# Optimization experiments

Hardware: AMD Instinct MI355X
Metric: run time of the kernel (lower is better)

Reference implementation:

```python
import jax, jax.numpy as jnp
import numpy as np

DIM = 1024
HID = 2048
E = 8      # num_experts
K = 2      # num_experts_per_tok
R = 16     # lora_rank
B_, S_ = 2, 1024


def setup_inputs() -> dict:
    key = jax.random.key(0)
    ks = jax.random.split(key, 14)
    n = lambda k, shape, scale: jax.random.normal(k, shape, jnp.float32) * scale
    inp = {
        "x": jax.random.normal(ks[0], (B_, S_, DIM), jnp.float32),
        "Wg": n(ks[1], (E, DIM), DIM ** -0.5),
        # w1: dim -> hidden (base weight, bias, lora A [r,in], lora B [out,r])
        "W1": n(ks[2], (E, HID, DIM), DIM ** -0.5),
        "b1": jnp.zeros((E, HID), jnp.float32),
        "A1": n(ks[3], (E, R, DIM), DIM ** -0.5),
        "B1": n(ks[4], (E, HID, R), 0.01),
        # w2: hidden -> dim
        "W2": n(ks[5], (E, DIM, HID), HID ** -0.5),
        "b2": jnp.zeros((E, DIM), jnp.float32),
        "A2": n(ks[6], (E, R, HID), HID ** -0.5),
        "B2": n(ks[7], (E, DIM, R), 0.01),
        # w3: dim -> hidden
        "W3": n(ks[8], (E, HID, DIM), DIM ** -0.5),
        "b3": jnp.zeros((E, HID), jnp.float32),
        "A3": n(ks[9], (E, R, DIM), DIM ** -0.5),
        "B3": n(ks[10], (E, HID, R), 0.01),
    }
    return inp


def _lora_in(xf, W, b, A, B):
    # xf: [T, D] shared input -> [T, E, H]; LoraLinear: x W^T + b + (x A^T) B^T
    base = jnp.einsum('td,ehd->teh', xf, W)
    low = jnp.einsum('ter,ehr->teh', jnp.einsum('td,erd->ter', xf, A), B)
    return base + low + b


def _lora_out(g, W, b, A, B):
    # g: [T, E, H] per-expert input -> [T, E, D]
    base = jnp.einsum('teh,edh->ted', g, W)
    low = jnp.einsum('ter,edr->ted', jnp.einsum('teh,erh->ter', g, A), B)
    return base + low + b


def reference(x, Wg, W1, b1, A1, B1, W2, b2, A2, B2, W3, b3, A3, B3):
    orig_shape = x.shape
    xf = x.reshape(-1, x.shape[-1])                      # [T, D]
    scores = jax.nn.softmax(xf @ Wg.T, axis=-1)          # [T, E]
    expert_weights, expert_indices = jax.lax.top_k(scores, K)
    expert_weights = expert_weights / expert_weights.sum(-1, keepdims=True)
    # sparse combine weights: zero for non-topk experts (== masked dispatch)
    gates = (jax.nn.one_hot(expert_indices, E, dtype=xf.dtype)
             * expert_weights[..., None]).sum(axis=1)    # [T, E]
    h1 = _lora_in(xf, W1, b1, A1, B1)                    # [T, E, H]
    h3 = _lora_in(xf, W3, b3, A3, B3)                    # [T, E, H]
    g = jax.nn.silu(h1) * h3                             # silu gating
    y_e = _lora_out(g, W2, b2, A2, B2)                   # [T, E, D]
    y = jnp.einsum('te,ted->td', gates, y_e)             # weighted combine
    return y.reshape(orig_shape)
```

## Files before the change

kernel.cpp:

```cpp
#include <hip/hip_runtime.h>

#define DIM 1024
#define HID 2048
#define NE 8
#define LR 16
#define T_TOK 2048
#define NROWS 4096
#define BM 128
#define BN 64
#define BK 64
#define MAX_MT 40
#define ROWS_PAD (NROWS + BM)

typedef __attribute__((ext_vector_type(8))) short bf16x8;
typedef __attribute__((ext_vector_type(4))) float f32x4;

__device__ __forceinline__ unsigned short f2bf(float f) {
  unsigned u = __builtin_bit_cast(unsigned, f);
  u += 0x7FFFu + ((u >> 16) & 1u);
  return (unsigned short)(u >> 16);
}

__device__ __forceinline__ void gload_lds16(const void* g, void* l) {
  __builtin_amdgcn_global_load_lds(
      (const __attribute__((address_space(1))) unsigned int*)g,
      (__attribute__((address_space(3))) unsigned int*)l, 16, 0, 0);
}

__global__ void routing_kernel(const float* __restrict__ x, const float* __restrict__ Wg,
                               int* __restrict__ counts, int* __restrict__ topk_idx,
                               float* __restrict__ topk_gate) {
  int t = blockIdx.x * 4 + (threadIdx.x >> 6);
  int lane = threadIdx.x & 63;
  const float* xr = x + (size_t)t * DIM;
  float xa[16];
#pragma unroll
  for (int i = 0; i < 16; i++) xa[i] = xr[lane + 64 * i];
  float lg[NE];
#pragma unroll
  for (int e = 0; e < NE; e++) {
    const float* wr_ = Wg + e * DIM;
    float s = 0.f;
#pragma unroll
    for (int i = 0; i < 16; i++) s += xa[i] * wr_[lane + 64 * i];
#pragma unroll
    for (int off = 32; off > 0; off >>= 1) s += __shfl_xor(s, off);
    lg[e] = s;
  }
  if (lane == 0) {
    int i0 = 0;
#pragma unroll
    for (int e = 1; e < NE; e++) if (lg[e] > lg[i0]) i0 = e;
    int i1 = (i0 == 0) ? 1 : 0;
#pragma unroll
    for (int e = 0; e < NE; e++) if (e != i0 && lg[e] > lg[i1]) i1 = e;
    float e1 = __expf(lg[i1] - lg[i0]);
    float inv = 1.f / (1.f + e1);
    topk_idx[2 * t] = i0;
    topk_idx[2 * t + 1] = i1;
    topk_gate[2 * t] = inv;
    topk_gate[2 * t + 1] = e1 * inv;
    atomicAdd(&counts[i0], 1);
    atomicAdd(&counts[i1], 1);
  }
}

__global__ void scan_kernel(const int* __restrict__ counts, int* __restrict__ offsets,
                            int* __restrict__ nmt, int* __restrict__ tiles) {
  if (threadIdx.x == 0) {
    int off = 0, nt = 0;
    for (int e = 0; e < NE; e++) {
      offsets[e] = off;
      int c = counts[e];
      for (int mm = 0; mm * BM < c; mm++) tiles[nt++] = (e << 16) | mm;
      off += c;
    }
    offsets[NE] = off;
    nmt[0] = nt;
  }
}

__global__ void scatter_kernel(const int* __restrict__ topk_idx,
                               const int* __restrict__ offsets, int* __restrict__ cursors,
                               int* __restrict__ perm, int* __restrict__ rowexp,
                               int* __restrict__ pos) {
  int i = blockIdx.x * 256 + threadIdx.x;
  int e = topk_idx[i];
  int r = offsets[e] + atomicAdd(&cursors[e], 1);
  perm[r] = i >> 1;
  rowexp[r] = e;
  pos[i] = r;
}

__global__ void gather_lora13_kernel(const float* __restrict__ x,
                                     const float* __restrict__ A1, const float* __restrict__ A3,
                                     const int* __restrict__ perm, const int* __restrict__ rowexp,
                                     unsigned short* __restrict__ Xg,
                                     float* __restrict__ t1g, float* __restrict__ t3g) {
  __shared__ float xs[DIM];
  int r = blockIdx.x;
  int t = perm[r], e = rowexp[r];
  int tid = threadIdx.x;
  float4 v = ((const float4*)(x + (size_t)t * DIM))[tid];
  ((float4*)xs)[tid] = v;
  ushort4 hv;
  hv.x = f2bf(v.x); hv.y = f2bf(v.y); hv.z = f2bf(v.z); hv.w = f2bf(v.w);
  ((ushort4*)(Xg + (size_t)r * DIM))[tid] = hv;
  __syncthreads();
  int w = tid >> 6, lane = tid & 63;
  const float* A = ((w < 2) ? A1 : A3) + (size_t)e * LR * DIM + (size_t)((w & 1) * 8) * DIM;
  float* tout = ((w < 2) ? t1g : t3g) + (size_t)r * LR + (w & 1) * 8;
  float acc[8];
#pragma unroll
  for (int j = 0; j < 8; j++) acc[j] = 0.f;
  for (int i = 0; i < 16; i++) {
    float xv = xs[lane + 64 * i];
#pragma unroll
    for (int j = 0; j < 8; j++) acc[j] += xv * A[(size_t)j * DIM + lane + 64 * i];
  }
#pragma unroll
  for (int j = 0; j < 8; j++) {
    float s = acc[j];
#pragma unroll
    for (int off = 32; off > 0; off >>= 1) s += __shfl_xor(s, off);
    if (lane == 0) tout[j] = s;
  }
}

__global__ void lora2_kernel(const unsigned short* __restrict__ gb,
                             const float* __restrict__ A2, const int* __restrict__ rowexp,
                             float* __restrict__ t2g) {
  __shared__ float gs[HID];
  int r = blockIdx.x, tid = threadIdx.x;
  int e = rowexp[r];
  uint4 raw = ((const uint4*)(gb + (size_t)r * HID))[tid];
  unsigned u[4] = {raw.x, raw.y, raw.z, raw.w};
#pragma unroll
  for (int k = 0; k < 4; k++) {
    gs[tid * 8 + 2 * k] = __builtin_bit_cast(float, u[k] << 16);
    gs[tid * 8 + 2 * k + 1] = __builtin_bit_cast(float, u[k] & 0xffff0000u);
  }
  __syncthreads();
  int w = tid >> 6, lane = tid & 63;
  const float* A = A2 + (size_t)e * LR * HID + (size_t)(w * 4) * HID;
  float acc[4];
#pragma unroll
  for (int j = 0; j < 4; j++) acc[j] = 0.f;
  for (int i = 0; i < HID / 64; i++) {
    float xv = gs[lane + 64 * i];
#pragma unroll
    for (int j = 0; j < 4; j++) acc[j] += xv * A[(size_t)j * HID + lane + 64 * i];
  }
#pragma unroll
  for (int j = 0; j < 4; j++) {
    float s = acc[j];
#pragma unroll
    for (int off = 32; off > 0; off >>= 1) s += __shfl_xor(s, off);
    if (lane == 0) t2g[(size_t)r * LR + w * 4 + j] = s;
  }
}

__global__ __launch_bounds__(256) void gemm1_dual(
    const unsigned short* __restrict__ Xg,
    const float* __restrict__ W1, const float* __restrict__ W3,
    const float* __restrict__ b1, const float* __restrict__ b3,
    const float* __restrict__ B1l, const float* __restrict__ B3l,
    const float* __restrict__ t1g, const float* __restrict__ t3g,
    const int* __restrict__ offsets, const int* __restrict__ nmt,
    const int* __restrict__ tiles,
    unsigned short* __restrict__ g) {
  int ntid = blockIdx.x & 31;
  int slot = blockIdx.x >> 5;
  if (slot >= nmt[0]) return;
  int tl = tiles[slot];
  int e = tl >> 16, mtile = tl & 0xffff;
  int row0 = offsets[e] + mtile * BM;
  int rowEnd = offsets[e + 1];
  int col0 = ntid * BN;

  __shared__ __align__(16) char smem[32768];
  unsigned short* As = (unsigned short*)smem;
  unsigned short* B1s = (unsigned short*)(smem + 16384);
  unsigned short* B3s = (unsigned short*)(smem + 24576);

  int tid = threadIdx.x, lane = tid & 63, w = tid >> 6;
  int wr = w >> 1, wc = w & 1;

  f32x4 acc1[4][2], acc3[4][2];
#pragma unroll
  for (int i = 0; i < 4; i++)
#pragma unroll
    for (int j = 0; j < 2; j++)
#pragma unroll
      for (int k = 0; k < 4; k++) { acc1[i][j][k] = 0.f; acc3[i][j][k] = 0.f; }

  const unsigned short* Ag = Xg + (size_t)row0 * DIM;
  const float* W1e = W1 + ((size_t)e * HID + col0) * DIM;
  const float* W3e = W3 + ((size_t)e * HID + col0) * DIM;

  for (int kt = 0; kt < DIM / BK; kt++) {
#pragma unroll
    for (int it = 0; it < 4; it++) {
      int rl = it * 32 + w * 8 + (lane >> 3);
      int cb = (lane & 7) * 8;
      gload_lds16(Ag + (size_t)rl * DIM + kt * BK + cb, As + (it * 32 + w * 8) * BK);
    }
#pragma unroll
    for (int it = 0; it < 4; it++) {
      int rl = it * 16 + (tid >> 4);
      int cs = (tid & 15) * 4;
      float4 f1 = *(const float4*)(W1e + (size_t)rl * DIM + kt * BK + cs);
      float4 f3 = *(const float4*)(W3e + (size_t)rl * DIM + kt * BK + cs);
      ushort4 h1, h3;
      h1.x = f2bf(f1.x); h1.y = f2bf(f1.y); h1.z = f2bf(f1.z); h1.w = f2bf(f1.w);
      h3.x = f2bf(f3.x); h3.y = f2bf(f3.y); h3.z = f2bf(f3.z); h3.w = f2bf(f3.w);
      *(ushort4*)(B1s + rl * BK + cs) = h1;
      *(ushort4*)(B3s + rl * BK + cs) = h3;
    }
    __syncthreads();
#pragma unroll
    for (int kk = 0; kk < 2; kk++) {
      bf16x8 a[4];
#pragma unroll
      for (int mm = 0; mm < 4; mm++)
        a[mm] = *(const bf16x8*)(As + (wr * 64 + mm * 16 + (lane & 15)) * BK + kk * 32 + (lane >> 4) * 8);
#pragma unroll
      for (int nn = 0; nn < 2; nn++) {
        bf16x8 bv1 = *(const bf16x8*)(B1s + (wc * 32 + nn * 16 + (lane & 15)) * BK + kk * 32 + (lane >> 4) * 8);
        bf16x8 bv3 = *(const bf16x8*)(B3s + (wc * 32 + nn * 16 + (lane & 15)) * BK + kk * 32 + (lane >> 4) * 8);
#pragma unroll
        for (int mm = 0; mm < 4; mm++) {
          acc1[mm][nn] = __builtin_amdgcn_mfma_f32_16x16x32_bf16(a[mm], bv1, acc1[mm][nn], 0, 0, 0);
          acc3[mm][nn] = __builtin_amdgcn_mfma_f32_16x16x32_bf16(a[mm], bv3, acc3[mm][nn], 0, 0, 0);
        }
      }
    }
    __syncthreads();
  }

  float* sT1 = (float*)smem;
  float* sT3 = sT1 + 128 * 17;
  float* sC1 = sT3 + 128 * 17;
  float* sC3 = sC1 + 64 * 17;
  float* sb1 = sC3 + 64 * 17;
  float* sb3 = sb1 + 64;
  for (int i = tid; i < 128 * 16; i += 256) {
    int rr = i >> 4, jj = i & 15;
    sT1[rr * 17 + jj] = t1g[(size_t)(row0 + rr) * LR + jj];
    sT3[rr * 17 + jj] = t3g[(size_t)(row0 + rr) * LR + jj];
  }
  for (int i = tid; i < 64 * 16; i += 256) {
    int rr = i >> 4, jj = i & 15;
    sC1[rr * 17 + jj] = B1l[((size_t)e * HID + col0 + rr) * LR + jj];
    sC3[rr * 17 + jj] = B3l[((size_t)e * HID + col0 + rr) * LR + jj];
  }
  if (tid < 64) {
    sb1[tid] = b1[e * HID + col0 + tid];
    sb3[tid] = b3[e * HID + col0 + tid];
  }
  __syncthreads();
#pragma unroll
  for (int mm = 0; mm < 4; mm++)
#pragma unroll
    for (int nn = 0; nn < 2; nn++) {
      int cl = wc * 32 + nn * 16 + (lane & 15);
      float bias1 = sb1[cl], bias3 = sb3[cl];
#pragma unroll
      for (int j = 0; j < 4; j++) {
        int rl = wr * 64 + mm * 16 + (lane >> 4) * 4 + j;
        float v1 = acc1[mm][nn][j] + bias1;
        float v3 = acc3[mm][nn][j] + bias3;
#pragma unroll
        for (int jj = 0; jj < 16; jj++) {
          v1 += sT1[rl * 17 + jj] * sC1[cl * 17 + jj];
          v3 += sT3[rl * 17 + jj] * sC3[cl * 17 + jj];
        }
        float gg = v1 * v3 / (1.f + __expf(-v1));
        int r = row0 + rl;
        if (r < rowEnd) g[(size_t)r * HID + col0 + cl] = f2bf(gg);
      }
    }
}

__global__ __launch_bounds__(256) void gemm2_kernel(
    const unsigned short* __restrict__ gb,
    const float* __restrict__ W2, const float* __restrict__ b2,
    const float* __restrict__ B2l, const float* __restrict__ t2g,
    const int* __restrict__ offsets, const int* __restrict__ nmt,
    const int* __restrict__ tiles,
    float* __restrict__ ye) {
  int ntid = blockIdx.x & 15;
  int slot = blockIdx.x >> 4;
  if (slot >= nmt[0]) return;
  int tl = tiles[slot];
  int e = tl >> 16, mtile = tl & 0xffff;
  int row0 = offsets[e] + mtile * BM;
  int rowEnd = offsets[e + 1];
  int col0 = ntid * BN;

  __shared__ __align__(16) char smem[24576];
  unsigned short* As = (unsigned short*)smem;
  unsigned short* Bs = (unsigned short*)(smem + 16384);

  int tid = threadIdx.x, lane = tid & 63, w = tid >> 6;
  int wr = w >> 1, wc = w & 1;

  f32x4 acc[4][2];
#pragma unroll
  for (int i = 0; i < 4; i++)
#pragma unroll
    for (int j = 0; j < 2; j++)
#pragma unroll
      for (int k = 0; k < 4; k++) acc[i][j][k] = 0.f;

  const unsigned short* Ag = gb + (size_t)row0 * HID;
  const float* W2e = W2 + ((size_t)e * DIM + col0) * HID;

  for (int kt = 0; kt < HID / BK; kt++) {
#pragma unroll
    for (int it = 0; it < 4; it++) {
      int rl = it * 32 + w * 8 + (lane >> 3);
      int cb = (lane & 7) * 8;
      gload_lds16(Ag + (size_t)rl * HID + kt * BK + cb, As + (it * 32 + w * 8) * BK);
    }
#pragma unroll
    for (int it = 0; it < 4; it++) {
      int rl = it * 16 + (tid >> 4);
      int cs = (tid & 15) * 4;
      float4 f = *(const float4*)(W2e + (size_t)rl * HID + kt * BK + cs);
      ushort4 h;
      h.x = f2bf(f.x); h.y = f2bf(f.y); h.z = f2bf(f.z); h.w = f2bf(f.w);
      *(ushort4*)(Bs + rl * BK + cs) = h;
    }
    __syncthreads();
#pragma unroll
    for (int kk = 0; kk < 2; kk++) {
      bf16x8 a[4];
#pragma unroll
      for (int mm = 0; mm < 4; mm++)
        a[mm] = *(const bf16x8*)(As + (wr * 64 + mm * 16 + (lane & 15)) * BK + kk * 32 + (lane >> 4) * 8);
#pragma unroll
      for (int nn = 0; nn < 2; nn++) {
        bf16x8 bv = *(const bf16x8*)(Bs + (wc * 32 + nn * 16 + (lane & 15)) * BK + kk * 32 + (lane >> 4) * 8);
#pragma unroll
        for (int mm = 0; mm < 4; mm++)
          acc[mm][nn] = __builtin_amdgcn_mfma_f32_16x16x32_bf16(a[mm], bv, acc[mm][nn], 0, 0, 0);
      }
    }
    __syncthreads();
  }

  float* sT2 = (float*)smem;
  float* sC2 = sT2 + 128 * 17;
  float* sb2 = sC2 + 64 * 17;
  for (int i = tid; i < 128 * 16; i += 256) {
    int rr = i >> 4, jj = i & 15;
    sT2[rr * 17 + jj] = t2g[(size_t)(row0 + rr) * LR + jj];
  }
  for (int i = tid; i < 64 * 16; i += 256) {
    int rr = i >> 4, jj = i & 15;
    sC2[rr * 17 + jj] = B2l[((size_t)e * DIM + col0 + rr) * LR + jj];
  }
  if (tid < 64) sb2[tid] = b2[e * DIM + col0 + tid];
  __syncthreads();
#pragma unroll
  for (int mm = 0; mm < 4; mm++)
#pragma unroll
    for (int nn = 0; nn < 2; nn++) {
      int cl = wc * 32 + nn * 16 + (lane & 15);
      float bias = sb2[cl];
#pragma unroll
      for (int j = 0; j < 4; j++) {
        int rl = wr * 64 + mm * 16 + (lane >> 4) * 4 + j;
        float v = acc[mm][nn][j] + bias;
#pragma unroll
        for (int jj = 0; jj < 16; jj++) v += sT2[rl * 17 + jj] * sC2[cl * 17 + jj];
        int r = row0 + rl;
        if (r < rowEnd) ye[(size_t)r * DIM + col0 + cl] = v;
      }
    }
}

__global__ void combine_kernel(const float* __restrict__ ye, const int* __restrict__ pos,
                               const float* __restrict__ topk_gate,
                               float* __restrict__ out) {
  int t = blockIdx.x, tid = threadIdx.x;
  int r0 = pos[2 * t], r1 = pos[2 * t + 1];
  float w0 = topk_gate[2 * t], w1 = topk_gate[2 * t + 1];
  float4 a = ((const float4*)(ye + (size_t)r0 * DIM))[tid];
  float4 b = ((const float4*)(ye + (size_t)r1 * DIM))[tid];
  float4 o;
  o.x = w0 * a.x + w1 * b.x;
  o.y = w0 * a.y + w1 * b.y;
  o.z = w0 * a.z + w1 * b.z;
  o.w = w0 * a.w + w1 * b.w;
  ((float4*)(out + (size_t)t * DIM))[tid] = o;
}

extern "C" void kernel_launch(void* const* d_in, const int* in_sizes, int n_in,
                              void* d_out, int out_size, void* d_ws, size_t ws_size,
                              hipStream_t stream) {
  (void)in_sizes; (void)n_in; (void)out_size; (void)ws_size;
  const float* x  = (const float*)d_in[0];
  const float* Wg = (const float*)d_in[1];
  const float* W1 = (const float*)d_in[2];
  const float* b1 = (const float*)d_in[3];
  const float* A1 = (const float*)d_in[4];
  const float* B1 = (const float*)d_in[5];
  const float* W2 = (const float*)d_in[6];
  const float* b2 = (const float*)d_in[7];
  const float* A2 = (const float*)d_in[8];
  const float* B2 = (const float*)d_in[9];
  const float* W3 = (const float*)d_in[10];
  const float* b3 = (const float*)d_in[11];
  const float* A3 = (const float*)d_in[12];
  const float* B3 = (const float*)d_in[13];
  float* out = (float*)d_out;

  char* ws = (char*)d_ws;
  int* counts   = (int*)ws;
  int* cursors  = counts + 8;
  int* offsets  = cursors + 8;
  int* nmt      = offsets + 9;
  int* tiles    = nmt + 1;
  int* topk_idx = (int*)(ws + 512);
  float* topk_gate = (float*)(ws + 512 + 16384);
  int* perm   = (int*)(ws + 512 + 2 * 16384);
  int* rowexp = (int*)(ws + 512 + 3 * 16384);
  int* pos    = (int*)(ws + 512 + 4 * 16384);
  size_t off = 82432;
  unsigned short* Xg = (unsigned short*)(ws + off); off += (size_t)ROWS_PAD * DIM * 2;
  unsigned short* gb = (unsigned short*)(ws + off); off += (size_t)ROWS_PAD * HID * 2;
  float* t1g = (float*)(ws + off); off += (size_t)ROWS_PAD * LR * 4;
  float* t3g = (float*)(ws + off); off += (size_t)ROWS_PAD * LR * 4;
  float* t2g = (float*)(ws + off); off += (size_t)ROWS_PAD * LR * 4;
  float* ye  = (float*)(ws + off); off += (size_t)NROWS * DIM * 4;

  hipMemsetAsync(d_ws, 0, 512, stream);
  routing_kernel<<<T_TOK / 4, 256, 0, stream>>>(x, Wg, counts, topk_idx, topk_gate);
  scan_kernel<<<1, 64, 0, stream>>>(counts, offsets, nmt, tiles);
  scatter_kernel<<<NROWS / 256, 256, 0, stream>>>(topk_idx, offsets, cursors, perm, rowexp, pos);
  gather_lora13_kernel<<<NROWS, 256, 0, stream>>>(x, A1, A3, perm, rowexp, Xg, t1g, t3g);
  gemm1_dual<<<MAX_MT * (HID / BN), 256, 0, stream>>>(Xg, W1, W3, b1, b3, B1, B3, t1g, t3g,
                                                      offsets, nmt, tiles, gb);
  lora2_kernel<<<NROWS, 256, 0, stream>>>(gb, A2, rowexp, t2g);
  gemm2_kernel<<<MAX_MT * (DIM / BN), 256, 0, stream>>>(gb, W2, b2, B2, t2g,
                                                        offsets, nmt, tiles, ye);
  combine_kernel<<<T_TOK, 256, 0, stream>>>(ye, pos, topk_gate, out);
}
```

Baseline: 690.1 us.

## Pre-convert expert weights to bf16 and double-buffer swizzled LDS loads in GEMMs

Adds a conversion kernel that turns W1, W3 and W2 into bf16 copies in the workspace every call. The two expert GEMMs can then stream weights directly into LDS with global_load_lds instead of converting them in registers. Both GEMMs become double-buffered with an XOR swizzle on the LDS layout, so the next tile loads while the current one computes and bank conflicts drop. The cost is an extra full read and write pass over all three weight tensors each call, plus twice the LDS per block, which may lower occupancy.

```diff
diff --git a/kernel.cpp b/kernel.cpp
--- a/kernel.cpp
+++ b/kernel.cpp
@@ -11,6 +11,7 @@
 #define BK 64
 #define MAX_MT 40
 #define ROWS_PAD (NROWS + BM)
+#define WELEMS (NE * HID * DIM)
 
 typedef __attribute__((ext_vector_type(8))) short bf16x8;
 typedef __attribute__((ext_vector_type(4))) float f32x4;
@@ -25,6 +26,18 @@
   __builtin_amdgcn_global_load_lds(
       (const __attribute__((address_space(1))) unsigned int*)g,
       (__attribute__((address_space(3))) unsigned int*)l, 16, 0, 0);
+}
+
+__global__ void wconv_kernel(const float* __restrict__ f, unsigned short* __restrict__ o, int n) {
+  for (int i = (blockIdx.x * 256 + threadIdx.x) * 8; i < n; i += gridDim.x * 256 * 8) {
+    float4 a = *(const float4*)(f + i);
+    float4 b = *(const float4*)(f + i + 4);
+    ushort4 h0, h1;
+    h0.x = f2bf(a.x); h0.y = f2bf(a.y); h0.z = f2bf(a.z); h0.w = f2bf(a.w);
+    h1.x = f2bf(b.x); h1.y = f2bf(b.y); h1.z = f2bf(b.z); h1.w = f2bf(b.w);
+    *(ushort4*)(o + i) = h0;
+    *(ushort4*)(o + i + 4) = h1;
+  }
 }
 
 __global__ void routing_kernel(const float* __restrict__ x, const float* __restrict__ Wg,
@@ -162,7 +175,7 @@
 
 __global__ __launch_bounds__(256) void gemm1_dual(
     const unsigned short* __restrict__ Xg,
-    const float* __restrict__ W1, const float* __restrict__ W3,
+    const unsigned short* __restrict__ W1b, const unsigned short* __restrict__ W3b,
     const float* __restrict__ b1, const float* __restrict__ b3,
     const float* __restrict__ B1l, const float* __restrict__ B3l,
     const float* __restrict__ t1g, const float* __restrict__ t3g,
@@ -178,13 +191,13 @@
   int rowEnd = offsets[e + 1];
   int col0 = ntid * BN;
 
-  __shared__ __align__(16) char smem[32768];
-  unsigned short* As = (unsigned short*)smem;
-  unsigned short* B1s = (unsigned short*)(smem + 16384);
-  unsigned short* B3s = (unsigned short*)(smem + 24576);
+  __shared__ __align__(16) char smem[65536];
 
   int tid = threadIdx.x, lane = tid & 63, w = tid >> 6;
   int wr = w >> 1, wc = w & 1;
+  int srow = lane >> 3;
+  int sperm = ((lane & 7) ^ srow) * 8;
+  int lxor = (lane & 7) << 3;
 
   f32x4 acc1[4][2], acc3[4][2];
 #pragma unroll
@@ -195,47 +208,56 @@
       for (int k = 0; k < 4; k++) { acc1[i][j][k] = 0.f; acc3[i][j][k] = 0.f; }
 
   const unsigned short* Ag = Xg + (size_t)row0 * DIM;
-  const float* W1e = W1 + ((size_t)e * HID + col0) * DIM;
-  const float* W3e = W3 + ((size_t)e * HID + col0) * DIM;
-
-  for (int kt = 0; kt < DIM / BK; kt++) {
-#pragma unroll
-    for (int it = 0; it < 4; it++) {
-      int rl = it * 32 + w * 8 + (lane >> 3);
-      int cb = (lane & 7) * 8;
-      gload_lds16(Ag + (size_t)rl * DIM + kt * BK + cb, As + (it * 32 + w * 8) * BK);
-    }
-#pragma unroll
-    for (int it = 0; it < 4; it++) {
-      int rl = it * 16 + (tid >> 4);
-      int cs = (tid & 15) * 4;
-      float4 f1 = *(const float4*)(W1e + (size_t)rl * DIM + kt * BK + cs);
-      float4 f3 = *(const float4*)(W3e + (size_t)rl * DIM + kt * BK + cs);
-      ushort4 h1, h3;
-      h1.x = f2bf(f1.x); h1.y = f2bf(f1.y); h1.z = f2bf(f1.z); h1.w = f2bf(f1.w);
-      h3.x = f2bf(f3.x); h3.y = f2bf(f3.y); h3.z = f2bf(f3.z); h3.w = f2bf(f3.w);
-      *(ushort4*)(B1s + rl * BK + cs) = h1;
-      *(ushort4*)(B3s + rl * BK + cs) = h3;
-    }
-    __syncthreads();
-#pragma unroll
-    for (int kk = 0; kk < 2; kk++) {
-      bf16x8 a[4];
-#pragma unroll
-      for (int mm = 0; mm < 4; mm++)
-        a[mm] = *(const bf16x8*)(As + (wr * 64 + mm * 16 + (lane & 15)) * BK + kk * 32 + (lane >> 4) * 8);
-#pragma unroll
-      for (int nn = 0; nn < 2; nn++) {
-        bf16x8 bv1 = *(const bf16x8*)(B1s + (wc * 32 + nn * 16 + (lane & 15)) * BK + kk * 32 + (lane >> 4) * 8);
-        bf16x8 bv3 = *(const bf16x8*)(B3s + (wc * 32 + nn * 16 + (lane & 15)) * BK + kk * 32 + (lane >> 4) * 8);
-#pragma unroll
-        for (int mm = 0; mm < 4; mm++) {
-          acc1[mm][nn] = __builtin_amdgcn_mfma_f32_16x16x32_bf16(a[mm], bv1, acc1[mm][nn], 0, 0, 0);
-          acc3[mm][nn] = __builtin_amdgcn_mfma_f32_16x16x32_bf16(a[mm], bv3, acc3[mm][nn], 0, 0, 0);
+  const unsigned short* W1e = W1b + ((size_t)e * HID + col0) * DIM;
+  const unsigned short* W3e = W3b + ((size_t)e * HID + col0) * DIM;
+
+#define STAGE1(buf, kt) { \
+    char* base_ = smem + (buf) * 32768; \
+    unsigned short* As_ = (unsigned short*)base_; \
+    unsigned short* B1s_ = (unsigned short*)(base_ + 16384); \
+    unsigned short* B3s_ = (unsigned short*)(base_ + 24576); \
+    int kc_ = (kt) * BK + sperm; \
+    _Pragma("unroll") \
+    for (int it = 0; it < 4; it++) \
+      gload_lds16(Ag + (size_t)(it * 32 + w * 8 + srow) * DIM + kc_, As_ + (it * 32 + w * 8) * BK); \
+    _Pragma("unroll") \
+    for (int it = 0; it < 2; it++) { \
+      gload_lds16(W1e + (size_t)(it * 32 + w * 8 + srow) * DIM + kc_, B1s_ + (it * 32 + w * 8) * BK); \
+      gload_lds16(W3e + (size_t)(it * 32 + w * 8 + srow) * DIM + kc_, B3s_ + (it * 32 + w * 8) * BK); \
+    } }
+
+  STAGE1(0, 0);
+  __syncthreads();
+  int cur = 0;
+  const int NT1 = DIM / BK;
+  for (int kt = 0; kt < NT1; kt++) {
+    if (kt + 1 < NT1) STAGE1(cur ^ 1, kt + 1);
+    {
+      char* base_ = smem + cur * 32768;
+      const unsigned short* As_ = (const unsigned short*)base_;
+      const unsigned short* B1s_ = (const unsigned short*)(base_ + 16384);
+      const unsigned short* B3s_ = (const unsigned short*)(base_ + 24576);
+#pragma unroll
+      for (int kk = 0; kk < 2; kk++) {
+        int kx = (kk * 32 + (lane >> 4) * 8) ^ lxor;
+        bf16x8 a[4];
+#pragma unroll
+        for (int mm = 0; mm < 4; mm++)
+          a[mm] = *(const bf16x8*)(As_ + (wr * 64 + mm * 16 + (lane & 15)) * BK + kx);
+#pragma unroll
+        for (int nn = 0; nn < 2; nn++) {
+          bf16x8 bv1 = *(const bf16x8*)(B1s_ + (wc * 32 + nn * 16 + (lane & 15)) * BK + kx);
+          bf16x8 bv3 = *(const bf16x8*)(B3s_ + (wc * 32 + nn * 16 + (lane & 15)) * BK + kx);
+#pragma unroll
+          for (int mm = 0; mm < 4; mm++) {
+            acc1[mm][nn] = __builtin_amdgcn_mfma_f32_16x16x32_bf16(a[mm], bv1, acc1[mm][nn], 0, 0, 0);
+            acc3[mm][nn] = __builtin_amdgcn_mfma_f32_16x16x32_bf16(a[mm], bv3, acc3[mm][nn], 0, 0, 0);
+          }
         }
       }
     }
     __syncthreads();
+    cur ^= 1;
   }
 
   float* sT1 = (float*)smem;
@@ -284,7 +306,7 @@
 
 __global__ __launch_bounds__(256) void gemm2_kernel(
     const unsigned short* __restrict__ gb,
-    const float* __restrict__ W2, const float* __restrict__ b2,
+    const unsigned short* __restrict__ W2b, const float* __restrict__ b2,
     const float* __restrict__ B2l, const float* __restrict__ t2g,
     const int* __restrict__ offsets, const int* __restrict__ nmt,
     const int* __restrict__ tiles,
@@ -298,12 +320,13 @@
   int rowEnd = offsets[e + 1];
   int col0 = ntid * BN;
 
-  __shared__ __align__(16) char smem[24576];
-  unsigned short* As = (unsigned short*)smem;
-  unsigned short* Bs = (unsigned short*)(smem + 16384);
+  __shared__ __align__(16) char smem[49152];
 
   int tid = threadIdx.x, lane = tid & 63, w = tid >> 6;
   int wr = w >> 1, wc = w & 1;
+  int srow = lane >> 3;
+  int sperm = ((lane & 7) ^ srow) * 8;
+  int lxor = (lane & 7) << 3;
 
   f32x4 acc[4][2];
 #pragma unroll
@@ -314,40 +337,49 @@
       for (int k = 0; k < 4; k++) acc[i][j][k] = 0.f;
 
   const unsigned short* Ag = gb + (size_t)row0 * HID;
-  const float* W2e = W2 + ((size_t)e * DIM + col0) * HID;
-
-  for (int kt = 0; kt < HID / BK; kt++) {
-#pragma unroll
-    for (int it = 0; it < 4; it++) {
-      int rl = it * 32 + w * 8 + (lane >> 3);
-      int cb = (lane & 7) * 8;
-      gload_lds16(Ag + (size_t)rl * HID + kt * BK + cb, As + (it * 32 + w * 8) * BK);
-    }
-#pragma unroll
-    for (int it = 0; it < 4; it++) {
-      int rl = it * 16 + (tid >> 4);
-      int cs = (tid & 15) * 4;
-      float4 f = *(const float4*)(W2e + (size_t)rl * HID + kt * BK + cs);
-      ushort4 h;
-      h.x = f2bf(f.x); h.y = f2bf(f.y); h.z = f2bf(f.z); h.w = f2bf(f.w);
-      *(ushort4*)(Bs + rl * BK + cs) = h;
+  const unsigned short* W2e = W2b + ((size_t)e * DIM + col0) * HID;
+
+#define STAGE2(buf, kt) { \
+    char* base_ = smem + (buf) * 24576; \
+    unsigned short* As_ = (unsigned short*)base_; \
+    unsigned short* Bs_ = (unsigned short*)(base_ + 16384); \
+    int kc_ = (kt) * BK + sperm; \
+    _Pragma("unroll") \
+    for (int it = 0; it < 4; it++) \
+      gload_lds16(Ag + (size_t)(it * 32 + w * 8 + srow) * HID + kc_, As_ + (it * 32 + w * 8) * BK); \
+    _Pragma("unroll") \
+    for (int it = 0; it < 2; it++) \
+      gload_lds16(W2e + (size_t)(it * 32 + w * 8 + srow) * HID + kc_, Bs_ + (it * 32 + w * 8) * BK); \
+    }
+
+  STAGE2(0, 0);
+  __syncthreads();
+  int cur = 0;
+  const int NT2 = HID / BK;
+  for (int kt = 0; kt < NT2; kt++) {
+    if (kt + 1 < NT2) STAGE2(cur ^ 1, kt + 1);
+    {
+      char* base_ = smem + cur * 24576;
+      const unsigned short* As_ = (const unsigned short*)base_;
+      const unsigned short* Bs_ = (const unsigned short*)(base_ + 16384);
+#pragma unroll
+      for (int kk = 0; kk < 2; kk++) {
+        int kx = (kk * 32 + (lane >> 4) * 8) ^ lxor;
+        bf16x8 a[4];
+#pragma unroll
+        for (int mm = 0; mm < 4; mm++)
+          a[mm] = *(const bf16x8*)(As_ + (wr * 64 + mm * 16 + (lane & 15)) * BK + kx);
+#pragma unroll
+        for (int nn = 0; nn < 2; nn++) {
+          bf16x8 bv = *(const bf16x8*)(Bs_ + (wc * 32 + nn * 16 + (lane & 15)) * BK + kx);
+#pragma unroll
+          for (int mm = 0; mm < 4; mm++)
+            acc[mm][nn] = __builtin_amdgcn_mfma_f32_16x16x32_bf16(a[mm], bv, acc[mm][nn], 0, 0, 0);
+        }
+      }
     }
     __syncthreads();
-#pragma unroll
-    for (int kk = 0; kk < 2; kk++) {
-      bf16x8 a[4];
-#pragma unroll
-      for (int mm = 0; mm < 4; mm++)
-        a[mm] = *(const bf16x8*)(As + (wr * 64 + mm * 16 + (lane & 15)) * BK + kk * 32 + (lane >> 4) * 8);
-#pragma unroll
-      for (int nn = 0; nn < 2; nn++) {
-        bf16x8 bv = *(const bf16x8*)(Bs + (wc * 32 + nn * 16 + (lane & 15)) * BK + kk * 32 + (lane >> 4) * 8);
-#pragma unroll
-        for (int mm = 0; mm < 4; mm++)
-          acc[mm][nn] = __builtin_amdgcn_mfma_f32_16x16x32_bf16(a[mm], bv, acc[mm][nn], 0, 0, 0);
-      }
-    }
-    __syncthreads();
+    cur ^= 1;
   }
 
   float* sT2 = (float*)smem;
@@ -435,16 +467,22 @@
   float* t3g = (float*)(ws + off); off += (size_t)ROWS_PAD * LR * 4;
   float* t2g = (float*)(ws + off); off += (size_t)ROWS_PAD * LR * 4;
   float* ye  = (float*)(ws + off); off += (size_t)NROWS * DIM * 4;
+  unsigned short* W1b = (unsigned short*)(ws + off); off += (size_t)WELEMS * 2;
+  unsigned short* W3b = (unsigned short*)(ws + off); off += (size_t)WELEMS * 2;
+  unsigned short* W2b = (unsigned short*)(ws + off); off += (size_t)WELEMS * 2;
 
   hipMemsetAsync(d_ws, 0, 512, stream);
+  wconv_kernel<<<4096, 256, 0, stream>>>(W1, W1b, WELEMS);
+  wconv_kernel<<<4096, 256, 0, stream>>>(W3, W3b, WELEMS);
+  wconv_kernel<<<4096, 256, 0, stream>>>(W2, W2b, WELEMS);
   routing_kernel<<<T_TOK / 4, 256, 0, stream>>>(x, Wg, counts, topk_idx, topk_gate);
   scan_kernel<<<1, 64, 0, stream>>>(counts, offsets, nmt, tiles);
   scatter_kernel<<<NROWS / 256, 256, 0, stream>>>(topk_idx, offsets, cursors, perm, rowexp, pos);
   gather_lora13_kernel<<<NROWS, 256, 0, stream>>>(x, A1, A3, perm, rowexp, Xg, t1g, t3g);
-  gemm1_dual<<<MAX_MT * (HID / BN), 256, 0, stream>>>(Xg, W1, W3, b1, b3, B1, B3, t1g, t3g,
+  gemm1_dual<<<MAX_MT * (HID / BN), 256, 0, stream>>>(Xg, W1b, W3b, b1, b3, B1, B3, t1g, t3g,
                                                       offsets, nmt, tiles, gb);
   lora2_kernel<<<NROWS, 256, 0, stream>>>(gb, A2, rowexp, t2g);
-  gemm2_kernel<<<MAX_MT * (DIM / BN), 256, 0, stream>>>(gb, W2, b2, B2, t2g,
+  gemm2_kernel<<<MAX_MT * (DIM / BN), 256, 0, stream>>>(gb, W2b, b2, B2, t2g,
                                                         offsets, nmt, tiles, ye);
   combine_kernel<<<T_TOK, 256, 0, stream>>>(ye, pos, topk_gate, out);
 }
```

After: 599.9 us. 13.1% less time.

## Pre-convert expert weights to bf16 and load them directly into swizzled LDS

Applied to the files above, without the earlier changes.

Adds a kernel that converts W1, W2 and W3 to bf16 once per call. The grouped GEMMs then stream bf16 weights with direct global-to-LDS loads instead of loading fp32, converting in registers and storing to LDS. It also applies an XOR swizzle to the LDS layout to reduce bank conflicts, and sets launch bounds to 4 blocks per CU. The conversion pass reads all fp32 weights (about 200 MB) and writes bf16 copies on every call. Each GEMM tile re-reads its weights many times across M tiles, so halving those bytes and dropping the conversion work may or may not outweigh the extra pass.

```diff
diff --git a/kernel.cpp b/kernel.cpp
--- a/kernel.cpp
+++ b/kernel.cpp
@@ -11,6 +11,7 @@
 #define BK 64
 #define MAX_MT 40
 #define ROWS_PAD (NROWS + BM)
+#define WELEMS (NE * HID * DIM)
 
 typedef __attribute__((ext_vector_type(8))) short bf16x8;
 typedef __attribute__((ext_vector_type(4))) float f32x4;
@@ -25,6 +26,26 @@
   __builtin_amdgcn_global_load_lds(
       (const __attribute__((address_space(1))) unsigned int*)g,
       (__attribute__((address_space(3))) unsigned int*)l, 16, 0, 0);
+}
+
+__global__ void wconv3_kernel(const float* __restrict__ W1, const float* __restrict__ W2,
+                              const float* __restrict__ W3,
+                              unsigned short* __restrict__ o1, unsigned short* __restrict__ o2,
+                              unsigned short* __restrict__ o3) {
+  for (long long i = (long long)(blockIdx.x * 256 + threadIdx.x) * 8; i < 3LL * WELEMS;
+       i += (long long)gridDim.x * 256 * 8) {
+    int which = (int)(i / WELEMS);
+    int idx = (int)(i - (long long)which * WELEMS);
+    const float* f = (which == 0) ? W1 : (which == 1) ? W2 : W3;
+    unsigned short* o = (which == 0) ? o1 : (which == 1) ? o2 : o3;
+    float4 a = *(const float4*)(f + idx);
+    float4 b = *(const float4*)(f + idx + 4);
+    ushort4 h0, h1;
+    h0.x = f2bf(a.x); h0.y = f2bf(a.y); h0.z = f2bf(a.z); h0.w = f2bf(a.w);
+    h1.x = f2bf(b.x); h1.y = f2bf(b.y); h1.z = f2bf(b.z); h1.w = f2bf(b.w);
+    *(ushort4*)(o + idx) = h0;
+    *(ushort4*)(o + idx + 4) = h1;
+  }
 }
 
 __global__ void routing_kernel(const float* __restrict__ x, const float* __restrict__ Wg,
@@ -160,9 +181,9 @@
   }
 }
 
-__global__ __launch_bounds__(256) void gemm1_dual(
+__global__ __launch_bounds__(256, 4) void gemm1_dual(
     const unsigned short* __restrict__ Xg,
-    const float* __restrict__ W1, const float* __restrict__ W3,
+    const unsigned short* __restrict__ W1b, const unsigned short* __restrict__ W3b,
     const float* __restrict__ b1, const float* __restrict__ b3,
     const float* __restrict__ B1l, const float* __restrict__ B3l,
     const float* __restrict__ t1g, const float* __restrict__ t3g,
@@ -185,6 +206,9 @@
 
   int tid = threadIdx.x, lane = tid & 63, w = tid >> 6;
   int wr = w >> 1, wc = w & 1;
+  int srow = lane >> 3;
+  int sperm = ((lane & 7) ^ srow) * 8;
+  int lxor = (lane & 7) << 3;
 
   f32x4 acc1[4][2], acc3[4][2];
 #pragma unroll
@@ -195,39 +219,32 @@
       for (int k = 0; k < 4; k++) { acc1[i][j][k] = 0.f; acc3[i][j][k] = 0.f; }
 
   const unsigned short* Ag = Xg + (size_t)row0 * DIM;
-  const float* W1e = W1 + ((size_t)e * HID + col0) * DIM;
-  const float* W3e = W3 + ((size_t)e * HID + col0) * DIM;
-
-  for (int kt = 0; kt < DIM / BK; kt++) {
-#pragma unroll
-    for (int it = 0; it < 4; it++) {
-      int rl = it * 32 + w * 8 + (lane >> 3);
-      int cb = (lane & 7) * 8;
-      gload_lds16(Ag + (size_t)rl * DIM + kt * BK + cb, As + (it * 32 + w * 8) * BK);
-    }
-#pragma unroll
-    for (int it = 0; it < 4; it++) {
-      int rl = it * 16 + (tid >> 4);
-      int cs = (tid & 15) * 4;
-      float4 f1 = *(const float4*)(W1e + (size_t)rl * DIM + kt * BK + cs);
-      float4 f3 = *(const float4*)(W3e + (size_t)rl * DIM + kt * BK + cs);
-      ushort4 h1, h3;
-      h1.x = f2bf(f1.x); h1.y = f2bf(f1.y); h1.z = f2bf(f1.z); h1.w = f2bf(f1.w);
-      h3.x = f2bf(f3.x); h3.y = f2bf(f3.y); h3.z = f2bf(f3.z); h3.w = f2bf(f3.w);
-      *(ushort4*)(B1s + rl * BK + cs) = h1;
-      *(ushort4*)(B3s + rl * BK + cs) = h3;
+  const unsigned short* W1e = W1b + ((size_t)e * HID + col0) * DIM;
+  const unsigned short* W3e = W3b + ((size_t)e * HID + col0) * DIM;
+
+  const int NT1 = DIM / BK;
+  for (int kt = 0; kt < NT1; kt++) {
+    int kc = kt * BK + sperm;
+#pragma unroll
+    for (int it = 0; it < 4; it++)
+      gload_lds16(Ag + (size_t)(it * 32 + w * 8 + srow) * DIM + kc, As + (it * 32 + w * 8) * BK);
+#pragma unroll
+    for (int it = 0; it < 2; it++) {
+      gload_lds16(W1e + (size_t)(it * 32 + w * 8 + srow) * DIM + kc, B1s + (it * 32 + w * 8) * BK);
+      gload_lds16(W3e + (size_t)(it * 32 + w * 8 + srow) * DIM + kc, B3s + (it * 32 + w * 8) * BK);
     }
     __syncthreads();
 #pragma unroll
     for (int kk = 0; kk < 2; kk++) {
+      int kx = (kk * 32 + (lane >> 4) * 8) ^ lxor;
       bf16x8 a[4];
 #pragma unroll
       for (int mm = 0; mm < 4; mm++)
-        a[mm] = *(const bf16x8*)(As + (wr * 64 + mm * 16 + (lane & 15)) * BK + kk * 32 + (lane >> 4) * 8);
+        a[mm] = *(const bf16x8*)(As + (wr * 64 + mm * 16 + (lane & 15)) * BK + kx);
 #pragma unroll
       for (int nn = 0; nn < 2; nn++) {
-        bf16x8 bv1 = *(const bf16x8*)(B1s + (wc * 32 + nn * 16 + (lane & 15)) * BK + kk * 32 + (lane >> 4) * 8);
-        bf16x8 bv3 = *(const bf16x8*)(B3s + (wc * 32 + nn * 16 + (lane & 15)) * BK + kk * 32 + (lane >> 4) * 8);
+        bf16x8 bv1 = *(const bf16x8*)(B1s + (wc * 32 + nn * 16 + (lane & 15)) * BK + kx);
+        bf16x8 bv3 = *(const bf16x8*)(B3s + (wc * 32 + nn * 16 + (lane & 15)) * BK + kx);
 #pragma unroll
         for (int mm = 0; mm < 4; mm++) {
           acc1[mm][nn] = __builtin_amdgcn_mfma_f32_16x16x32_bf16(a[mm], bv1, acc1[mm][nn], 0, 0, 0);
@@ -282,9 +299,9 @@
     }
 }
 
-__global__ __launch_bounds__(256) void gemm2_kernel(
+__global__ __launch_bounds__(256, 4) void gemm2_kernel(
     const unsigned short* __restrict__ gb,
-    const float* __restrict__ W2, const float* __restrict__ b2,
+    const unsigned short* __restrict__ W2b, const float* __restrict__ b2,
     const float* __restrict__ B2l, const float* __restrict__ t2g,
     const int* __restrict__ offsets, const int* __restrict__ nmt,
     const int* __restrict__ tiles,
@@ -304,6 +321,9 @@
 
   int tid = threadIdx.x, lane = tid & 63, w = tid >> 6;
   int wr = w >> 1, wc = w & 1;
+  int srow = lane >> 3;
+  int sperm = ((lane & 7) ^ srow) * 8;
+  int lxor = (lane & 7) << 3;
 
   f32x4 acc[4][2];
 #pragma unroll
@@ -314,34 +334,28 @@
       for (int k = 0; k < 4; k++) acc[i][j][k] = 0.f;
 
   const unsigned short* Ag = gb + (size_t)row0 * HID;
-  const float* W2e = W2 + ((size_t)e * DIM + col0) * HID;
-
-  for (int kt = 0; kt < HID / BK; kt++) {
-#pragma unroll
-    for (int it = 0; it < 4; it++) {
-      int rl = it * 32 + w * 8 + (lane >> 3);
-      int cb = (lane & 7) * 8;
-      gload_lds16(Ag + (size_t)rl * HID + kt * BK + cb, As + (it * 32 + w * 8) * BK);
-    }
-#pragma unroll
-    for (int it = 0; it < 4; it++) {
-      int rl = it * 16 + (tid >> 4);
-      int cs = (tid & 15) * 4;
-      float4 f = *(const float4*)(W2e + (size_t)rl * HID + kt * BK + cs);
-      ushort4 h;
-      h.x = f2bf(f.x); h.y = f2bf(f.y); h.z = f2bf(f.z); h.w = f2bf(f.w);
-      *(ushort4*)(Bs + rl * BK + cs) = h;
-    }
+  const unsigned short* W2e = W2b + ((size_t)e * DIM + col0) * HID;
+
+  const int NT2 = HID / BK;
+  for (int kt = 0; kt < NT2; kt++) {
+    int kc = kt * BK + sperm;
+#pragma unroll
+    for (int it = 0; it < 4; it++)
+      gload_lds16(Ag + (size_t)(it * 32 + w * 8 + srow) * HID + kc, As + (it * 32 + w * 8) * BK);
+#pragma unroll
+    for (int it = 0; it < 2; it++)
+      gload_lds16(W2e + (size_t)(it * 32 + w * 8 + srow) * HID + kc, Bs + (it * 32 + w * 8) * BK);
     __syncthreads();
 #pragma unroll
     for (int kk = 0; kk < 2; kk++) {
+      int kx = (kk * 32 + (lane >> 4) * 8) ^ lxor;
       bf16x8 a[4];
 #pragma unroll
       for (int mm = 0; mm < 4; mm++)
-        a[mm] = *(const bf16x8*)(As + (wr * 64 + mm * 16 + (lane & 15)) * BK + kk * 32 + (lane >> 4) * 8);
+        a[mm] = *(const bf16x8*)(As + (wr * 64 + mm * 16 + (lane & 15)) * BK + kx);
 #pragma unroll
       for (int nn = 0; nn < 2; nn++) {
-        bf16x8 bv = *(const bf16x8*)(Bs + (wc * 32 + nn * 16 + (lane & 15)) * BK + kk * 32 + (lane >> 4) * 8);
+        bf16x8 bv = *(const bf16x8*)(Bs + (wc * 32 + nn * 16 + (lane & 15)) * BK + kx);
 #pragma unroll
         for (int mm = 0; mm < 4; mm++)
           acc[mm][nn] = __builtin_amdgcn_mfma_f32_16x16x32_bf16(a[mm], bv, acc[mm][nn], 0, 0, 0);
@@ -435,16 +449,20 @@
   float* t3g = (float*)(ws + off); off += (size_t)ROWS_PAD * LR * 4;
   float* t2g = (float*)(ws + off); off += (size_t)ROWS_PAD * LR * 4;
   float* ye  = (float*)(ws + off); off += (size_t)NROWS * DIM * 4;
+  unsigned short* W1b = (unsigned short*)(ws + off); off += (size_t)WELEMS * 2;
+  unsigned short* W3b = (unsigned short*)(ws + off); off += (size_t)WELEMS * 2;
+  unsigned short* W2b = (unsigned short*)(ws + off); off += (size_t)WELEMS * 2;
 
   hipMemsetAsync(d_ws, 0, 512, stream);
+  wconv3_kernel<<<8192, 256, 0, stream>>>(W1, W2, W3, W1b, W2b, W3b);
   routing_kernel<<<T_TOK / 4, 256, 0, stream>>>(x, Wg, counts, topk_idx, topk_gate);
   scan_kernel<<<1, 64, 0, stream>>>(counts, offsets, nmt, tiles);
   scatter_kernel<<<NROWS / 256, 256, 0, stream>>>(topk_idx, offsets, cursors, perm, rowexp, pos);
   gather_lora13_kernel<<<NROWS, 256, 0, stream>>>(x, A1, A3, perm, rowexp, Xg, t1g, t3g);
-  gemm1_dual<<<MAX_MT * (HID / BN), 256, 0, stream>>>(Xg, W1, W3, b1, b3, B1, B3, t1g, t3g,
+  gemm1_dual<<<MAX_MT * (HID / BN), 256, 0, stream>>>(Xg, W1b, W3b, b1, b3, B1, B3, t1g, t3g,
                                                       offsets, nmt, tiles, gb);
   lora2_kernel<<<NROWS, 256, 0, stream>>>(gb, A2, rowexp, t2g);
-  gemm2_kernel<<<MAX_MT * (DIM / BN), 256, 0, stream>>>(gb, W2, b2, B2, t2g,
+  gemm2_kernel<<<MAX_MT * (DIM / BN), 256, 0, stream>>>(gb, W2b, b2, B2, t2g,
                                                         offsets, nmt, tiles, ye);
   combine_kernel<<<T_TOK, 256, 0, stream>>>(ye, pos, topk_gate, out);
 }
```

After: 592.7 us. -14.1%, faster.
